# Kernel optimization log

Measured on AMD Instinct MI355X. Metric: run time of the kernel, lower is better.

The kernel has to match this reference:

```python
import jax, jax.numpy as jnp
import numpy as np

GROUP = 64  # group_size for precision='int4'


def setup_inputs() -> dict:
    key = jax.random.key(0)
    ks = jax.random.split(key, 7)
    B, S, C, O, R = 64, 4, 8192, 8192, 32
    x = jax.random.normal(ks[0], (B, S, C), dtype=jnp.float32)
    # unpacked int4 weight values stored as int32 codes in [0,16) -> value = code - 8
    qweight = jax.random.randint(ks[1], (O, C), 0, 16, dtype=jnp.int32)
    wscales = jax.random.uniform(ks[2], (C // GROUP, O), dtype=jnp.float32,
                                 minval=0.005, maxval=0.02)
    # smoothing factors kept strictly positive and away from zero
    smooth_factor = jax.random.uniform(ks[3], (C,), dtype=jnp.float32,
                                       minval=0.5, maxval=1.5)
    proj_down = jax.random.normal(ks[4], (C, R), dtype=jnp.float32) * 0.02
    proj_up = jax.random.normal(ks[5], (O, R), dtype=jnp.float32) * 0.02
    bias = jax.random.normal(ks[6], (O,), dtype=jnp.float32) * 0.01
    return {"x": x, "qweight": qweight, "wscales": wscales,
            "smooth_factor": smooth_factor, "proj_down": proj_down,
            "proj_up": proj_up, "bias": bias}


def reference(x, qweight, wscales, smooth_factor, proj_down, proj_up, bias):
    B, S, C = x.shape
    O = qweight.shape[0]
    ng = C // GROUP
    xr = x.reshape(B * S, C)

    # SVD low-rank correction: lora_act = x @ proj_down ; out += lora_act @ proj_up^T
    lora = (xr @ proj_down) @ proj_up.T  # (M, O)

    # activation smoothing + per-group symmetric int4 quantization
    xs = xr / smooth_factor                                   # (M, C)
    xg = xs.reshape(-1, ng, GROUP)                            # (M, ng, 64)
    ascales = jnp.max(jnp.abs(xg), axis=-1, keepdims=True) / 7.0
    ascales = jnp.maximum(ascales, 1e-8)
    q_act = jnp.clip(jnp.round(xg / ascales), -8.0, 7.0)
    x_deq = (q_act * ascales).reshape(-1, C)                  # dequantized act

    # per-group weight dequant: wscales is (ng, O)
    w = (qweight.astype(jnp.float32) - 8.0).reshape(O, ng, GROUP)
    w_deq = (w * wscales.T[:, :, None]).reshape(O, C)         # (O, C)

    out = x_deq @ w_deq.T + lora + bias                       # (M, O)
    return out.reshape(B, S, O)
```

## Files before the change

kernel.cpp:

```cpp
#include <hip/hip_runtime.h>
#include <stdint.h>

#define C_DIM 8192
#define O_DIM 8192
#define M_DIM 256
#define NG    128
#define RK    32

typedef float f32x4 __attribute__((ext_vector_type(4)));
typedef int   i32x4 __attribute__((ext_vector_type(4)));
typedef unsigned int u32;

__device__ __forceinline__ void gll4(const void* g, void* l) {
  __builtin_amdgcn_global_load_lds(
      (const __attribute__((address_space(1))) void*)g,
      (__attribute__((address_space(3))) void*)l, 4, 0, 0);
}

__global__ __launch_bounds__(256) void k_lora(const float* __restrict__ x,
                                              const float* __restrict__ pd,
                                              float* __restrict__ lact) {
  const int t  = threadIdx.x;
  const int rq = t & 7;
  const int kc = (t >> 3) & 15;
  const int ml = t >> 7;
  const int m  = blockIdx.x * 2 + ml;
  const float* xrow = x + (size_t)m * C_DIM + kc * 512;
  const float* pdp  = pd + (size_t)(kc * 512) * RK + rq * 4;
  float a0 = 0.f, a1 = 0.f, a2 = 0.f, a3 = 0.f;
  for (int k = 0; k < 512; k += 4) {
    float4 xv = *(const float4*)(xrow + k);
    float4 p0 = *(const float4*)(pdp + (size_t)(k + 0) * RK);
    float4 p1 = *(const float4*)(pdp + (size_t)(k + 1) * RK);
    float4 p2 = *(const float4*)(pdp + (size_t)(k + 2) * RK);
    float4 p3 = *(const float4*)(pdp + (size_t)(k + 3) * RK);
    a0 += xv.x * p0.x + xv.y * p1.x + xv.z * p2.x + xv.w * p3.x;
    a1 += xv.x * p0.y + xv.y * p1.y + xv.z * p2.y + xv.w * p3.y;
    a2 += xv.x * p0.z + xv.y * p1.z + xv.z * p2.z + xv.w * p3.z;
    a3 += xv.x * p0.w + xv.y * p1.w + xv.z * p2.w + xv.w * p3.w;
  }
  __shared__ float red[2][8][16][4];
  red[ml][rq][kc][0] = a0;
  red[ml][rq][kc][1] = a1;
  red[ml][rq][kc][2] = a2;
  red[ml][rq][kc][3] = a3;
  __syncthreads();
  if (t < 64) {
    const int ml2 = t >> 5, r = t & 31, rq2 = r >> 2, j = r & 3;
    float s = 0.f;
#pragma unroll
    for (int c = 0; c < 16; ++c) s += red[ml2][rq2][c][j];
    lact[(size_t)(blockIdx.x * 2 + ml2) * RK + r] = s;
  }
}

__global__ __launch_bounds__(256) void k_prep(const float* __restrict__ x,
                                              const float* __restrict__ smooth,
                                              float* __restrict__ scp3,
                                              i32x4* __restrict__ wsA8) {
  const int t    = threadIdx.x;
  const int ml   = t & 15;
  const int gl   = t >> 4;
  const int MT   = blockIdx.x >> 3;
  const int gblk = blockIdx.x & 7;
  const int m = MT * 16 + ml;
  const int g = gblk * 16 + gl;
  const float* xp = x + (size_t)m * C_DIM + g * 64;
  const float* sp = smooth + g * 64;
  float xs[64];
  float amax = 0.0f;
#pragma unroll
  for (int i = 0; i < 64; i += 4) {
    float4 xv = *(const float4*)(xp + i);
    float4 sv = *(const float4*)(sp + i);
    xs[i + 0] = xv.x / sv.x;
    xs[i + 1] = xv.y / sv.y;
    xs[i + 2] = xv.z / sv.z;
    xs[i + 3] = xv.w / sv.w;
    amax = fmaxf(amax, fabsf(xs[i + 0]));
    amax = fmaxf(amax, fabsf(xs[i + 1]));
    amax = fmaxf(amax, fabsf(xs[i + 2]));
    amax = fmaxf(amax, fabsf(xs[i + 3]));
  }
  const float ascale = fmaxf(amax / 7.0f, 1e-8f);
  int qi[64];
  int rs = 0;
#pragma unroll
  for (int i = 0; i < 64; ++i) {
    float qv = fminf(fmaxf(rintf(xs[i] / ascale), -8.0f), 7.0f);
    qi[i] = (int)qv;
    rs += qi[i];
  }
  const int h = m >> 7, mll = m & 127;
  scp3[((size_t)h * NG + g) * 256 + mll]       = ascale;
  scp3[((size_t)h * NG + g) * 256 + 128 + mll] = 8.0f * (float)rs * ascale;
  const size_t base = ((size_t)(MT * NG + g)) * 64;
#pragma unroll
  for (int lg = 0; lg < 4; ++lg) {
    const int* q = qi + lg * 16;
    i32x4 c;
#pragma unroll
    for (int dw = 0; dw < 4; ++dw)
      c[dw] = (q[dw * 4 + 0] & 0xff) | ((q[dw * 4 + 1] & 0xff) << 8) |
              ((q[dw * 4 + 2] & 0xff) << 16) | (q[dw * 4 + 3] << 24);
    wsA8[base + lg * 16 + ml] = c;
  }
}

__global__ __launch_bounds__(256, 4) void k_main(
    const int* __restrict__ qw, const float* __restrict__ wsc,
    const float* __restrict__ pu, const float* __restrict__ bias,
    const float* __restrict__ scp3, const i32x4* __restrict__ wsA8,
    const float* __restrict__ lact, float* __restrict__ out) {
  const int t    = threadIdx.x;
  const int bid  = blockIdx.x;
  const int mh   = bid & 1;
  const int n0   = (bid >> 1) * 16;
  const int w    = t >> 6;
  const int l    = t & 63;
  const int lrow = l >> 4;
  const int lcol = l & 15;

  __shared__ int   ldsBf[4 * 256];
  __shared__ float ldsSCf[4 * 256];
  __shared__ float ldsW[NG * 16];

  for (int i = t; i < NG * 16; i += 256)
    ldsW[i] = wsc[(size_t)(i >> 4) * O_DIM + n0 + (i & 15)];

  const int sr = t >> 4, cg = t & 15;
  const int* gB = qw + (size_t)(n0 + sr) * C_DIM + cg * 4;
  const int pwIdx = sr * 16 + (((cg >> 2) ^ ((sr >> 1) & 3)) << 2) + (cg & 3);
  const int rdIdx = lcol * 16 + ((lrow ^ ((lcol >> 1) & 3)) << 2);

  const float* gSC = scp3 + ((size_t)mh * NG) * 256 + t;
  const i32x4* gA0 = wsA8 + ((size_t)(mh * 8 + w * 2 + 0) * NG) * 64 + l;
  const i32x4* gA1 = wsA8 + ((size_t)(mh * 8 + w * 2 + 1) * NG) * 64 + l;

  const int scBase = w * 32 + lrow * 4;

  __syncthreads();

  i32x4 bR0, bR1, bR2, bR3;
  i32x4 A0_0, A0_1, A1_0, A1_1, A2_0, A2_1, A3_0, A3_1;

  bR0 = *(const i32x4*)(gB);
  gll4(gSC, &ldsSCf[0 * 256 + t]);
  A0_0 = gA0[0];
  A0_1 = gA1[0];
  asm volatile("" ::: "memory");
  bR1 = *(const i32x4*)(gB + 64);
  gll4(gSC + 256, &ldsSCf[1 * 256 + t]);
  A1_0 = gA0[64];
  A1_1 = gA1[64];
  asm volatile("" ::: "memory");
  bR2 = *(const i32x4*)(gB + 128);
  gll4(gSC + 512, &ldsSCf[2 * 256 + t]);
  A2_0 = gA0[128];
  A2_1 = gA1[128];

  f32x4 acc0 = (f32x4){0.f, 0.f, 0.f, 0.f};
  f32x4 acc1 = (f32x4){0.f, 0.f, 0.f, 0.f};
  const i32x4 z = (i32x4){0, 0, 0, 0};

#define BODY(U, UP3, G)                                                        \
  {                                                                            \
    asm volatile("s_waitcnt vmcnt(8) lgkmcnt(0)" ::: "memory");                \
    int pk = (bR##U[0] & 0xff) | ((bR##U[1] & 0xff) << 8) |                    \
             ((bR##U[2] & 0xff) << 16) | (bR##U[3] << 24);                     \
    ldsBf[(U) * 256 + pwIdx] = pk;                                             \
    asm volatile("s_waitcnt lgkmcnt(0)" ::: "memory");                         \
    __builtin_amdgcn_s_barrier();                                              \
    i32x4 bf = *(const i32x4*)&ldsBf[(U) * 256 + rdIdx];                       \
    f32x4 as0 = *(const f32x4*)&ldsSCf[(U) * 256 + scBase];                    \
    f32x4 rs0 = *(const f32x4*)&ldsSCf[(U) * 256 + scBase + 128];              \
    f32x4 as1 = *(const f32x4*)&ldsSCf[(U) * 256 + scBase + 16];               \
    f32x4 rs1 = *(const f32x4*)&ldsSCf[(U) * 256 + scBase + 144];              \
    const float wsv = ldsW[(G) * 16 + lcol];                                   \
    {                                                                          \
      int g3 = (G) + 3;                                                        \
      if (g3 > NG - 1) g3 = NG - 1;                                            \
      bR##UP3 = *(const i32x4*)(gB + (size_t)g3 * 64);                         \
      gll4(gSC + (size_t)g3 * 256, &ldsSCf[(UP3) * 256 + t]);                  \
      A##UP3##_0 = gA0[(size_t)g3 * 64];                                       \
      A##UP3##_1 = gA1[(size_t)g3 * 64];                                       \
    }                                                                          \
    i32x4 d0 = __builtin_amdgcn_mfma_i32_16x16x64_i8(A##U##_0, bf, z, 0, 0, 0);\
    i32x4 d1 = __builtin_amdgcn_mfma_i32_16x16x64_i8(A##U##_1, bf, z, 0, 0, 0);\
    f32x4 df0, df1;                                                            \
    df0[0] = (float)d0[0]; df0[1] = (float)d0[1];                              \
    df0[2] = (float)d0[2]; df0[3] = (float)d0[3];                              \
    df1[0] = (float)d1[0]; df1[1] = (float)d1[1];                              \
    df1[2] = (float)d1[2]; df1[3] = (float)d1[3];                              \
    acc0 += wsv * (as0 * df0 - rs0);                                           \
    acc1 += wsv * (as1 * df1 - rs1);                                           \
  }

  for (int p = 0; p < NG / 4; ++p) {
    const int g0 = p * 4;
    BODY(0, 3, g0 + 0)
    BODY(1, 0, g0 + 1)
    BODY(2, 1, g0 + 2)
    BODY(3, 2, g0 + 3)
  }
#undef BODY

  const int n = n0 + lcol;
  const float bv = bias[n];
  float4 puq[8];
#pragma unroll
  for (int rq = 0; rq < 8; ++rq)
    puq[rq] = *(const float4*)(pu + (size_t)n * RK + rq * 4);
#pragma unroll
  for (int mi = 0; mi < 2; ++mi) {
    const f32x4 av = (mi == 0) ? acc0 : acc1;
#pragma unroll
    for (int j = 0; j < 4; ++j) {
      const int m = mh * 128 + (w * 2 + mi) * 16 + lrow * 4 + j;
      const float* lp = lact + (size_t)m * RK;
      float lo = 0.f;
#pragma unroll
      for (int rq = 0; rq < 8; ++rq) {
        float4 lv = *(const float4*)(lp + rq * 4);
        lo += lv.x * puq[rq].x + lv.y * puq[rq].y + lv.z * puq[rq].z +
              lv.w * puq[rq].w;
      }
      out[(size_t)m * O_DIM + n] = av[j] + bv + lo;
    }
  }
}

extern "C" void kernel_launch(void* const* d_in, const int* in_sizes, int n_in,
                              void* d_out, int out_size, void* d_ws,
                              size_t ws_size, hipStream_t stream) {
  const float* x      = (const float*)d_in[0];
  const int*   qw     = (const int*)d_in[1];
  const float* wsc    = (const float*)d_in[2];
  const float* smooth = (const float*)d_in[3];
  const float* pd     = (const float*)d_in[4];
  const float* pu     = (const float*)d_in[5];
  const float* bias   = (const float*)d_in[6];
  float* out = (float*)d_out;

  char* ws = (char*)d_ws;
  float* lact = (float*)ws;
  float* scp3 = (float*)(ws + 32 * 1024);
  i32x4* wsA8 = (i32x4*)(ws + 288 * 1024);

  hipLaunchKernelGGL(k_prep, dim3(128), dim3(256), 0, stream, x, smooth, scp3,
                     wsA8);
  hipLaunchKernelGGL(k_lora, dim3(128), dim3(256), 0, stream, x, pd, lact);
  hipLaunchKernelGGL(k_main, dim3(1024), dim3(256), 0, stream, qw, wsc, pu,
                     bias, scp3, wsA8, lact, out);
}
```

Baseline: 192.0 us.

## Cover all rows per block, double-buffer 8-group weight super-stages

The main kernel now uses 512-thread blocks that each cover all 256 rows for a 16-column slice, instead of splitting rows across two blocks. Each int4 weight tile is therefore loaded from global memory once rather than twice. Weights are loaded in 8-group super-stages with 16-byte nontemporal loads, packed into a double-buffered, XOR-swizzled LDS tile, and synchronised with one barrier per super-stage instead of one per group. Activation scales are relaid out so they can be fetched with 16-byte global-to-LDS loads. The cost is more LDS per block, higher register pressure and the risk of occupancy limits at the larger block size.

```diff
diff --git a/kernel.cpp b/kernel.cpp
--- a/kernel.cpp
+++ b/kernel.cpp
@@ -6,15 +6,21 @@
 #define M_DIM 256
 #define NG    128
 #define RK    32
+#define SUPS  16
+#define GPS   8
 
 typedef float f32x4 __attribute__((ext_vector_type(4)));
 typedef int   i32x4 __attribute__((ext_vector_type(4)));
 typedef unsigned int u32;
 
-__device__ __forceinline__ void gll4(const void* g, void* l) {
+__device__ __forceinline__ void gll16(const void* g, void* l) {
   __builtin_amdgcn_global_load_lds(
       (const __attribute__((address_space(1))) void*)g,
-      (__attribute__((address_space(3))) void*)l, 4, 0, 0);
+      (__attribute__((address_space(3))) void*)l, 16, 0, 0);
+}
+__device__ __forceinline__ int pack8(i32x4 r) {
+  return (r[0] & 0xff) | ((r[1] & 0xff) << 8) | ((r[2] & 0xff) << 16) |
+         (r[3] << 24);
 }
 
 __global__ __launch_bounds__(256) void k_lora(const float* __restrict__ x,
@@ -56,7 +62,7 @@
 
 __global__ __launch_bounds__(256) void k_prep(const float* __restrict__ x,
                                               const float* __restrict__ smooth,
-                                              float* __restrict__ scp3,
+                                              float* __restrict__ scp,
                                               i32x4* __restrict__ wsA8) {
   const int t    = threadIdx.x;
   const int ml   = t & 15;
@@ -91,9 +97,8 @@
     qi[i] = (int)qv;
     rs += qi[i];
   }
-  const int h = m >> 7, mll = m & 127;
-  scp3[((size_t)h * NG + g) * 256 + mll]       = ascale;
-  scp3[((size_t)h * NG + g) * 256 + 128 + mll] = 8.0f * (float)rs * ascale;
+  scp[(size_t)g * 512 + m]       = ascale;
+  scp[(size_t)g * 512 + 256 + m] = 8.0f * (float)rs * ascale;
   const size_t base = ((size_t)(MT * NG + g)) * 64;
 #pragma unroll
   for (int lg = 0; lg < 4; ++lg) {
@@ -107,86 +112,79 @@
   }
 }
 
-__global__ __launch_bounds__(256, 4) void k_main(
+__global__ __launch_bounds__(512, 4) void k_main(
     const int* __restrict__ qw, const float* __restrict__ wsc,
     const float* __restrict__ pu, const float* __restrict__ bias,
-    const float* __restrict__ scp3, const i32x4* __restrict__ wsA8,
+    const float* __restrict__ scp, const i32x4* __restrict__ wsA8,
     const float* __restrict__ lact, float* __restrict__ out) {
   const int t    = threadIdx.x;
-  const int bid  = blockIdx.x;
-  const int mh   = bid & 1;
-  const int n0   = (bid >> 1) * 16;
+  const int n0   = blockIdx.x * 16;
   const int w    = t >> 6;
   const int l    = t & 63;
   const int lrow = l >> 4;
   const int lcol = l & 15;
 
-  __shared__ int   ldsBf[4 * 256];
-  __shared__ float ldsSCf[4 * 256];
+  __shared__ char  ldsB[2][16][512];
+  __shared__ float ldsSC[2][4096];
   __shared__ float ldsW[NG * 16];
 
-  for (int i = t; i < NG * 16; i += 256)
+  for (int i = t; i < NG * 16; i += 512)
     ldsW[i] = wsc[(size_t)(i >> 4) * O_DIM + n0 + (i & 15)];
 
-  const int sr = t >> 4, cg = t & 15;
-  const int* gB = qw + (size_t)(n0 + sr) * C_DIM + cg * 4;
-  const int pwIdx = sr * 16 + (((cg >> 2) ^ ((sr >> 1) & 3)) << 2) + (cg & 3);
-  const int rdIdx = lcol * 16 + ((lrow ^ ((lcol >> 1) & 3)) << 2);
-
-  const float* gSC = scp3 + ((size_t)mh * NG) * 256 + t;
-  const i32x4* gA0 = wsA8 + ((size_t)(mh * 8 + w * 2 + 0) * NG) * 64 + l;
-  const i32x4* gA1 = wsA8 + ((size_t)(mh * 8 + w * 2 + 1) * NG) * 64 + l;
-
-  const int scBase = w * 32 + lrow * 4;
-
-  __syncthreads();
-
-  i32x4 bR0, bR1, bR2, bR3;
-  i32x4 A0_0, A0_1, A1_0, A1_1, A2_0, A2_1, A3_0, A3_1;
-
-  bR0 = *(const i32x4*)(gB);
-  gll4(gSC, &ldsSCf[0 * 256 + t]);
-  A0_0 = gA0[0];
-  A0_1 = gA1[0];
-  asm volatile("" ::: "memory");
-  bR1 = *(const i32x4*)(gB + 64);
-  gll4(gSC + 256, &ldsSCf[1 * 256 + t]);
-  A1_0 = gA0[64];
-  A1_1 = gA1[64];
-  asm volatile("" ::: "memory");
-  bR2 = *(const i32x4*)(gB + 128);
-  gll4(gSC + 512, &ldsSCf[2 * 256 + t]);
-  A2_0 = gA0[128];
-  A2_1 = gA1[128];
+  const int sr = t >> 5, cg = t & 31;
+  const int* gB = qw + (size_t)(n0 + sr) * C_DIM + cg * 16;
+  const int wslot = (cg ^ (sr & 7)) * 16;
+  const char* gSCb = (const char*)scp;
+  const i32x4* gA0 = wsA8 + ((size_t)(w * 2 + 0) * NG) * 64 + l;
+  const i32x4* gA1 = wsA8 + ((size_t)(w * 2 + 1) * NG) * 64 + l;
 
   f32x4 acc0 = (f32x4){0.f, 0.f, 0.f, 0.f};
   f32x4 acc1 = (f32x4){0.f, 0.f, 0.f, 0.f};
   const i32x4 z = (i32x4){0, 0, 0, 0};
 
-#define BODY(U, UP3, G)                                                        \
+  i32x4 br0, br1, br2, br3;
+  i32x4 R0_0, R0_1, R1_0, R1_1, R2_0, R2_1, R3_0, R3_1;
+
+  __syncthreads();
+
+  br0 = __builtin_nontemporal_load((const i32x4*)(gB + 0));
+  br1 = __builtin_nontemporal_load((const i32x4*)(gB + 4));
+  br2 = __builtin_nontemporal_load((const i32x4*)(gB + 8));
+  br3 = __builtin_nontemporal_load((const i32x4*)(gB + 12));
+  gll16(gSCb + t * 16, &ldsSC[0][t * 4]);
+  gll16(gSCb + 8192 + t * 16, &ldsSC[0][2048 + t * 4]);
+  R0_0 = gA0[0 * 64];  R0_1 = gA1[0 * 64];
+  R1_0 = gA0[1 * 64];  R1_1 = gA1[1 * 64];
+  R2_0 = gA0[2 * 64];  R2_1 = gA1[2 * 64];
+  R3_0 = gA0[3 * 64];  R3_1 = gA1[3 * 64];
+  asm volatile("s_waitcnt vmcnt(8)" ::: "memory");
+  {
+    i32x4 pk = (i32x4){pack8(br0), pack8(br1), pack8(br2), pack8(br3)};
+    *(i32x4*)&ldsB[0][sr][wslot] = pk;
+  }
+  asm volatile("s_waitcnt lgkmcnt(0)" ::: "memory");
+  __builtin_amdgcn_s_barrier();
+
+#define SUBJ(J, RA, RB, VMC)                                                   \
   {                                                                            \
-    asm volatile("s_waitcnt vmcnt(8) lgkmcnt(0)" ::: "memory");                \
-    int pk = (bR##U[0] & 0xff) | ((bR##U[1] & 0xff) << 8) |                    \
-             ((bR##U[2] & 0xff) << 16) | (bR##U[3] << 24);                     \
-    ldsBf[(U) * 256 + pwIdx] = pk;                                             \
-    asm volatile("s_waitcnt lgkmcnt(0)" ::: "memory");                         \
-    __builtin_amdgcn_s_barrier();                                              \
-    i32x4 bf = *(const i32x4*)&ldsBf[(U) * 256 + rdIdx];                       \
-    f32x4 as0 = *(const f32x4*)&ldsSCf[(U) * 256 + scBase];                    \
-    f32x4 rs0 = *(const f32x4*)&ldsSCf[(U) * 256 + scBase + 128];              \
-    f32x4 as1 = *(const f32x4*)&ldsSCf[(U) * 256 + scBase + 16];               \
-    f32x4 rs1 = *(const f32x4*)&ldsSCf[(U) * 256 + scBase + 144];              \
-    const float wsv = ldsW[(G) * 16 + lcol];                                   \
-    {                                                                          \
-      int g3 = (G) + 3;                                                        \
-      if (g3 > NG - 1) g3 = NG - 1;                                            \
-      bR##UP3 = *(const i32x4*)(gB + (size_t)g3 * 64);                         \
-      gll4(gSC + (size_t)g3 * 256, &ldsSCf[(UP3) * 256 + t]);                  \
-      A##UP3##_0 = gA0[(size_t)g3 * 64];                                       \
-      A##UP3##_1 = gA1[(size_t)g3 * 64];                                       \
-    }                                                                          \
-    i32x4 d0 = __builtin_amdgcn_mfma_i32_16x16x64_i8(A##U##_0, bf, z, 0, 0, 0);\
-    i32x4 d1 = __builtin_amdgcn_mfma_i32_16x16x64_i8(A##U##_1, bf, z, 0, 0, 0);\
+    asm volatile("s_waitcnt vmcnt(" #VMC ")" ::: "memory");                    \
+    i32x4 bf = *(const i32x4*)&ldsB[s & 1][lcol]                               \
+                   [(((J) * 4 + lrow) ^ (lcol & 7)) * 16];                     \
+    f32x4 as0 = *(const f32x4*)&ldsSC[s & 1][(J) * 512 + (w * 2 + 0) * 16 +    \
+                                             lrow * 4];                        \
+    f32x4 rs0 = *(const f32x4*)&ldsSC[s & 1][(J) * 512 + 256 +                 \
+                                             (w * 2 + 0) * 16 + lrow * 4];     \
+    f32x4 as1 = *(const f32x4*)&ldsSC[s & 1][(J) * 512 + (w * 2 + 1) * 16 +    \
+                                             lrow * 4];                        \
+    f32x4 rs1 = *(const f32x4*)&ldsSC[s & 1][(J) * 512 + 256 +                 \
+                                             (w * 2 + 1) * 16 + lrow * 4];     \
+    const float wsv = ldsW[(s * GPS + (J)) * 16 + lcol];                       \
+    i32x4 d0 = __builtin_amdgcn_mfma_i32_16x16x64_i8(RA, bf, z, 0, 0, 0);      \
+    i32x4 d1 = __builtin_amdgcn_mfma_i32_16x16x64_i8(RB, bf, z, 0, 0, 0);      \
+    int gn = s * GPS + (J) + 4;                                                \
+    if (gn > NG - 1) gn = NG - 1;                                              \
+    RA = gA0[(size_t)gn * 64];                                                 \
+    RB = gA1[(size_t)gn * 64];                                                 \
     f32x4 df0, df1;                                                            \
     df0[0] = (float)d0[0]; df0[1] = (float)d0[1];                              \
     df0[2] = (float)d0[2]; df0[3] = (float)d0[3];                              \
@@ -196,14 +194,32 @@
     acc1 += wsv * (as1 * df1 - rs1);                                           \
   }
 
-  for (int p = 0; p < NG / 4; ++p) {
-    const int g0 = p * 4;
-    BODY(0, 3, g0 + 0)
-    BODY(1, 0, g0 + 1)
-    BODY(2, 1, g0 + 2)
-    BODY(3, 2, g0 + 3)
-  }
-#undef BODY
+  for (int s = 0; s < SUPS; ++s) {
+    const int sn = (s < SUPS - 1) ? s + 1 : SUPS - 1;
+    const int nb = (s + 1) & 1;
+    br0 = __builtin_nontemporal_load((const i32x4*)(gB + sn * 512 + 0));
+    br1 = __builtin_nontemporal_load((const i32x4*)(gB + sn * 512 + 4));
+    br2 = __builtin_nontemporal_load((const i32x4*)(gB + sn * 512 + 8));
+    br3 = __builtin_nontemporal_load((const i32x4*)(gB + sn * 512 + 12));
+    gll16(gSCb + (size_t)sn * 16384 + t * 16, &ldsSC[nb][t * 4]);
+    gll16(gSCb + (size_t)sn * 16384 + 8192 + t * 16, &ldsSC[nb][2048 + t * 4]);
+
+    SUBJ(0, R0_0, R0_1, 12)
+    SUBJ(1, R1_0, R1_1, 12)
+    SUBJ(2, R2_0, R2_1, 12)
+    SUBJ(3, R3_0, R3_1, 12)
+    SUBJ(4, R0_0, R0_1, 6)
+    SUBJ(5, R1_0, R1_1, 6)
+    SUBJ(6, R2_0, R2_1, 6)
+    SUBJ(7, R3_0, R3_1, 6)
+
+    asm volatile("s_waitcnt vmcnt(8)" ::: "memory");
+    i32x4 pk = (i32x4){pack8(br0), pack8(br1), pack8(br2), pack8(br3)};
+    *(i32x4*)&ldsB[nb][sr][wslot] = pk;
+    asm volatile("s_waitcnt lgkmcnt(0)" ::: "memory");
+    __builtin_amdgcn_s_barrier();
+  }
+#undef SUBJ
 
   const int n = n0 + lcol;
   const float bv = bias[n];
@@ -216,7 +232,7 @@
     const f32x4 av = (mi == 0) ? acc0 : acc1;
 #pragma unroll
     for (int j = 0; j < 4; ++j) {
-      const int m = mh * 128 + (w * 2 + mi) * 16 + lrow * 4 + j;
+      const int m = (w * 2 + mi) * 16 + lrow * 4 + j;
       const float* lp = lact + (size_t)m * RK;
       float lo = 0.f;
 #pragma unroll
@@ -244,12 +260,12 @@
 
   char* ws = (char*)d_ws;
   float* lact = (float*)ws;
-  float* scp3 = (float*)(ws + 32 * 1024);
+  float* scp  = (float*)(ws + 32 * 1024);
   i32x4* wsA8 = (i32x4*)(ws + 288 * 1024);
 
-  hipLaunchKernelGGL(k_prep, dim3(128), dim3(256), 0, stream, x, smooth, scp3,
+  hipLaunchKernelGGL(k_prep, dim3(128), dim3(256), 0, stream, x, smooth, scp,
                      wsA8);
   hipLaunchKernelGGL(k_lora, dim3(128), dim3(256), 0, stream, x, pd, lact);
-  hipLaunchKernelGGL(k_main, dim3(1024), dim3(256), 0, stream, qw, wsc, pu,
-                     bias, scp3, wsA8, lact, out);
-}
+  hipLaunchKernelGGL(k_main, dim3(512), dim3(512), 0, stream, qw, wsc, pu,
+                     bias, scp, wsA8, lact, out);
+}
```

After: 163.5 us. 14.8% less time.
